# Kernel optimization log

Measured on AMD Instinct MI355X. Metric: run time of the kernel, lower is better.

The kernel has to match this reference:

```python
import jax, jax.numpy as jnp
import numpy as np

N, E, F, H, C, K = 100000, 1600000, 512, 256, 64, 10
EPS = 1e-5  # BatchNorm1d default eps


def setup_inputs() -> dict:
    key = jax.random.key(0)
    ks = jax.random.split(key, 8)
    x = jax.random.normal(ks[0], (N, F), jnp.float32)
    # edge list with no self-loops (gcn_norm adds the self-loops itself)
    src = jax.random.randint(ks[1], (E,), 0, N)
    off = jax.random.randint(ks[2], (E,), 1, N)
    dst = (src + off) % N
    edge_index = jnp.stack([src, dst])
    s = lambda k, sh: jax.random.normal(k, sh, jnp.float32) * 0.02
    W0 = s(ks[3], (F, H)); b0 = jnp.zeros((H,), jnp.float32)
    g0 = jnp.ones((H,), jnp.float32); be0 = jnp.zeros((H,), jnp.float32)
    W1 = s(ks[4], (H, H)); b1 = jnp.zeros((H,), jnp.float32)
    g1 = jnp.ones((H,), jnp.float32); be1 = jnp.zeros((H,), jnp.float32)
    W2 = s(ks[5], (H, C)); b2 = jnp.zeros((C,), jnp.float32)
    proj_w = s(ks[6], (C, 1)); proj_b = jnp.zeros((1,), jnp.float32)
    return dict(x=x, W0=W0, b0=b0, g0=g0, be0=be0, W1=W1, b1=b1, g1=g1,
                be1=be1, W2=W2, b2=b2, proj_w=proj_w, proj_b=proj_b,
                edge_index=edge_index)


def _batchnorm(h, gamma, beta):
    # training-mode BN over the node (batch) axis, biased variance like torch
    mu = h.mean(0)
    var = h.var(0)
    return gamma * (h - mu) * jax.lax.rsqrt(var + EPS) + beta


def _prop(x, edge_index, proj_w, proj_b):
    n, c = x.shape
    loop = jnp.arange(n, dtype=edge_index.dtype)
    row = jnp.concatenate([edge_index[0], loop])  # message sources (x_j)
    col = jnp.concatenate([edge_index[1], loop])  # aggregation targets
    w = jnp.ones(row.shape, x.dtype)
    deg = jax.ops.segment_sum(w, col, num_segments=n)
    dis = jnp.where(deg > 0, jax.lax.rsqrt(jnp.maximum(deg, 1.0)) * (deg > 0), 0.0)
    dis = jnp.where(deg > 0, deg ** -0.5, 0.0)
    norm = dis[row] * dis[col]  # symmetric GCN normalization per edge

    def hop(xk, _):
        msgs = norm[:, None] * xk[row]               # gather + scale  [E+N, C]
        xk = jax.ops.segment_sum(msgs, col, num_segments=n)  # scatter-add
        return xk, xk

    _, hops = jax.lax.scan(hop, x, None, length=K)   # [K, N, C]
    pps = jnp.concatenate([x[None], hops], axis=0).transpose(1, 0, 2)  # [N, K+1, C]
    score = jax.nn.sigmoid(pps @ proj_w + proj_b)[..., 0]  # [N, K+1]
    return jnp.einsum('nk,nkc->nc', score, pps)      # [N, C]


def reference(x, W0, b0, g0, be0, W1, b1, g1, be1, W2, b2, proj_w, proj_b,
              edge_index):
    h = jax.nn.relu(_batchnorm(x @ W0 + b0, g0, be0))   # dropout is identity (eval)
    h = jax.nn.relu(_batchnorm(h @ W1 + b1, g1, be1))
    h = h @ W2 + b2                                     # [N, C] logits
    out = _prop(h, edge_index, proj_w, proj_b)
    return jax.nn.log_softmax(out, axis=1)
```

## Files before the change

### kernel.cpp

```cpp
#include <hip/hip_runtime.h>
#include <hip/hip_bf16.h>
#include <math.h>

#define NN 100000
#define FF 512
#define HH 256
#define CC 64
#define KHOPS 10
#define BN_EPS 1e-5f

typedef __bf16 bf16x8 __attribute__((ext_vector_type(8)));
typedef float f32x4 __attribute__((ext_vector_type(4)));
typedef unsigned short ushort8v __attribute__((ext_vector_type(8)));

__device__ __forceinline__ unsigned short f2bf(float f) {
    __bf16 b = (__bf16)f;
    return __builtin_bit_cast(unsigned short, b);
}
__device__ __forceinline__ float bf2f(unsigned short h) {
    unsigned u = ((unsigned)h) << 16;
    return __builtin_bit_cast(float, u);
}

typedef __attribute__((address_space(1))) const void g_void;
typedef __attribute__((address_space(3))) void l_void;
__device__ __forceinline__ void gl2lds16(const void* g, void* l) {
    __builtin_amdgcn_global_load_lds((g_void*)g, (l_void*)l, 16, 0, 0);
}

__global__ void k_zero(float* p, int n) {
    int i = blockIdx.x * blockDim.x + threadIdx.x;
    if (i < n) p[i] = 0.f;
}

__global__ void k_deg_init(int* deg, int n) {
    int i = blockIdx.x * blockDim.x + threadIdx.x;
    if (i < n) deg[i] = 1;
}

__global__ void k_deg_count(const int* __restrict__ dst, int e, int* deg) {
    for (int i = blockIdx.x * blockDim.x + threadIdx.x; i < e; i += gridDim.x * blockDim.x)
        atomicAdd(&deg[dst[i]], 1);
}

__global__ void k_dis(const int* __restrict__ deg, float* dis, int n) {
    int i = blockIdx.x * blockDim.x + threadIdx.x;
    if (i < n) dis[i] = rsqrtf((float)deg[i]);
}

#define SCAN_B 1024
#define SCAN_NB ((NN + SCAN_B - 1) / SCAN_B)

__global__ void k_scan1(const int* __restrict__ deg, int* __restrict__ part, int n) {
    __shared__ int ls[SCAN_B];
    int i = blockIdx.x * SCAN_B + threadIdx.x;
    ls[threadIdx.x] = (i < n) ? deg[i] - 1 : 0;
    __syncthreads();
    for (int d = SCAN_B / 2; d > 0; d >>= 1) {
        if (threadIdx.x < d) ls[threadIdx.x] += ls[threadIdx.x + d];
        __syncthreads();
    }
    if (threadIdx.x == 0) part[blockIdx.x] = ls[0];
}

__global__ void k_scan2(int* part, int* offs_last, int nb) {
    if (threadIdx.x == 0) {
        int run = 0;
        for (int b = 0; b < nb; b++) { int v = part[b]; part[b] = run; run += v; }
        offs_last[0] = run;
    }
}

__global__ void k_scan3(const int* __restrict__ deg, const int* __restrict__ part,
                        int* __restrict__ offs, int* __restrict__ cur, int n) {
    __shared__ int ls[SCAN_B];
    int i = blockIdx.x * SCAN_B + threadIdx.x;
    int v = (i < n) ? deg[i] - 1 : 0;
    ls[threadIdx.x] = v;
    __syncthreads();
    for (int d = 1; d < SCAN_B; d <<= 1) {
        int t = (threadIdx.x >= d) ? ls[threadIdx.x - d] : 0;
        __syncthreads();
        ls[threadIdx.x] += t;
        __syncthreads();
    }
    if (i < n) {
        int ex = part[blockIdx.x] + ls[threadIdx.x] - v;
        offs[i] = ex;
        cur[i] = ex;
    }
}

__global__ void k_fill(const int* __restrict__ src, const int* __restrict__ dst, int e,
                       const float* __restrict__ dis, int* cursor,
                       int* __restrict__ csrc, float* __restrict__ cw) {
    for (int i = blockIdx.x * blockDim.x + threadIdx.x; i < e; i += gridDim.x * blockDim.x) {
        int d = dst[i];
        int s = src[i];
        int p = atomicAdd(&cursor[d], 1);
        csrc[p] = s;
        cw[p] = dis[s] * dis[d];
    }
}

__global__ void k_wt(const float* __restrict__ W, unsigned short* __restrict__ Wt,
                     int K, int N) {
    int i = blockIdx.x * blockDim.x + threadIdx.x;
    if (i < K * N) {
        int n = i / K;
        int k = i - n * K;
        Wt[i] = f2bf(W[(size_t)k * N + n]);
    }
}

template <int AF32, int BN_, int STATS>
__global__ __launch_bounds__(256) void k_gemm_mfma(
    const void* __restrict__ Av, const unsigned short* __restrict__ Bt,
    const float* __restrict__ bias, unsigned short* __restrict__ Cb,
    float* __restrict__ sum, float* __restrict__ sumsq,
    int M, int K, int Nd) {
    constexpr int NREP = BN_ / 32;
    constexpr int ACH = AF32 ? 8 : 4;
    constexpr int AOPS = AF32 ? 4 : 2;
    constexpr int ASZ = AF32 ? 16384 : 8192;
    __shared__ __align__(16) unsigned char Asb[ASZ];
    __shared__ __align__(16) unsigned char Bsb[BN_ * 64];
    const int tid = threadIdx.x;
    const int lane = tid & 63;
    const int wid = tid >> 6;
    const int wrow = wid >> 1, wcol = wid & 1;
    const int row_base = blockIdx.y * 128;
    const int col_base = blockIdx.x * BN_;
    const unsigned char* Abase = (const unsigned char*)Av;
    const size_t arowb = (size_t)K * (AF32 ? 4 : 2);

    f32x4 acc[4][NREP];
#pragma unroll
    for (int m = 0; m < 4; m++)
#pragma unroll
        for (int n = 0; n < NREP; n++)
#pragma unroll
            for (int j = 0; j < 4; j++) acc[m][n][j] = 0.f;

    for (int kt = 0; kt < K; kt += 32) {
#pragma unroll
        for (int i = 0; i < AOPS; ++i) {
            int e = i * 256 + tid;
            int r = e / ACH;
            int c = e % ACH;
            int cs = AF32 ? (c ^ (r & 7)) : (c ^ ((r >> 1) & 3));
            int grow = row_base + r;
            if (grow > M - 1) grow = M - 1;
            const void* g = Abase + (size_t)grow * arowb + (size_t)kt * (AF32 ? 4 : 2) + (cs << 4);
            gl2lds16(g, Asb + e * 16);
        }
#pragma unroll
        for (int i = 0; i < BN_ / 64; ++i) {
            int e = i * 256 + tid;
            int r = e >> 2, c = e & 3;
            int cs = c ^ ((r >> 1) & 3);
            const void* g = (const unsigned char*)Bt + (size_t)(col_base + r) * (K * 2) +
                            (size_t)kt * 2 + (cs << 4);
            gl2lds16(g, Bsb + e * 16);
        }
        __syncthreads();

        bf16x8 af[4], bfr[NREP];
#pragma unroll
        for (int m = 0; m < 4; ++m) {
            int r = wrow * 64 + m * 16 + (lane & 15);
            if (AF32) {
                int x7 = r & 7;
                int q2 = (lane >> 4) * 2;
                f32x4 f0 = *(const f32x4*)(Asb + r * 128 + ((q2 ^ x7) << 4));
                f32x4 f1 = *(const f32x4*)(Asb + r * 128 + (((q2 + 1) ^ x7) << 4));
                bf16x8 a;
                a[0] = (__bf16)f0[0]; a[1] = (__bf16)f0[1]; a[2] = (__bf16)f0[2]; a[3] = (__bf16)f0[3];
                a[4] = (__bf16)f1[0]; a[5] = (__bf16)f1[1]; a[6] = (__bf16)f1[2]; a[7] = (__bf16)f1[3];
                af[m] = a;
            } else {
                int cs = (lane >> 4) ^ ((r >> 1) & 3);
                af[m] = *(const bf16x8*)(Asb + r * 64 + (cs << 4));
            }
        }
#pragma unroll
        for (int n = 0; n < NREP; ++n) {
            int r = wcol * (BN_ / 2) + n * 16 + (lane & 15);
            int cs = (lane >> 4) ^ ((r >> 1) & 3);
            bfr[n] = *(const bf16x8*)(Bsb + r * 64 + (cs << 4));
        }
#pragma unroll
        for (int m = 0; m < 4; ++m)
#pragma unroll
            for (int n = 0; n < NREP; ++n)
                acc[m][n] = __builtin_amdgcn_mfma_f32_16x16x32_bf16(af[m], bfr[n], acc[m][n], 0, 0, 0);
        __syncthreads();
    }

    const int lc = lane & 15;
    const int lr = (lane >> 4) * 4;
#pragma unroll
    for (int m = 0; m < 4; ++m) {
        int gr0 = row_base + wrow * 64 + m * 16 + lr;
#pragma unroll
        for (int n = 0; n < NREP; ++n) {
            int gc = col_base + wcol * (BN_ / 2) + n * 16 + lc;
            float bb = bias[gc];
#pragma unroll
            for (int j = 0; j < 4; ++j) {
                int gr = gr0 + j;
                if (gr < M) Cb[(size_t)gr * Nd + gc] = f2bf(acc[m][n][j] + bb);
            }
        }
    }
    if (STATS) {
#pragma unroll
        for (int n = 0; n < NREP; ++n) {
            int gc = col_base + wcol * (BN_ / 2) + n * 16 + lc;
            float bb = bias[gc];
            float s = 0.f, s2 = 0.f;
#pragma unroll
            for (int m = 0; m < 4; ++m) {
                int gr0 = row_base + wrow * 64 + m * 16 + lr;
#pragma unroll
                for (int j = 0; j < 4; ++j) {
                    if (gr0 + j < M) {
                        float v = acc[m][n][j] + bb;
                        s += v;
                        s2 += v * v;
                    }
                }
            }
            s += __shfl_xor(s, 16); s += __shfl_xor(s, 32);
            s2 += __shfl_xor(s2, 16); s2 += __shfl_xor(s2, 32);
            if ((lane >> 4) == 0) {
                atomicAdd(&sum[gc], s);
                atomicAdd(&sumsq[gc], s2);
            }
        }
    }
}

__global__ void k_bnfin(const float* __restrict__ sum, const float* __restrict__ sq,
                        const float* __restrict__ g, const float* __restrict__ be,
                        float* scale, float* shift) {
    int c = threadIdx.x;
    float mu = sum[c] * (1.f / NN);
    float var = sq[c] * (1.f / NN) - mu * mu;
    float sc = g[c] * rsqrtf(var + BN_EPS);
    scale[c] = sc;
    shift[c] = be[c] - mu * sc;
}

__global__ void k_bnapply(unsigned short* __restrict__ h, const float* __restrict__ scale,
                          const float* __restrict__ shift, int n) {
    int total = n * 32;
    for (int idx = blockIdx.x * blockDim.x + threadIdx.x; idx < total;
         idx += gridDim.x * blockDim.x) {
        int c8 = (idx & 31) * 8;
        ushort8v v = *(ushort8v*)(h + (size_t)idx * 8);
        f32x4 s0 = *(const f32x4*)(scale + c8);
        f32x4 s1 = *(const f32x4*)(scale + c8 + 4);
        f32x4 h0 = *(const f32x4*)(shift + c8);
        f32x4 h1 = *(const f32x4*)(shift + c8 + 4);
#pragma unroll
        for (int j = 0; j < 4; j++) {
            v[j] = f2bf(fmaxf(bf2f(v[j]) * s0[j] + h0[j], 0.f));
            v[j + 4] = f2bf(fmaxf(bf2f(v[j + 4]) * s1[j] + h1[j], 0.f));
        }
        *(ushort8v*)(h + (size_t)idx * 8) = v;
    }
}

__global__ void k_hop(const unsigned short* __restrict__ xin,
                      unsigned short* __restrict__ xout,
                      const int* __restrict__ offs, const int* __restrict__ csrc,
                      const float* __restrict__ cw, const float* __restrict__ dis,
                      int n) {
    int wid = (int)((blockIdx.x * (size_t)blockDim.x + threadIdx.x) >> 6);
    if (wid >= n) return;
    int lane = threadIdx.x & 63;
    int q = lane >> 4;
    int l = lane & 15;
    const uint2* x8 = (const uint2*)xin;
    float y0 = 0.f, y1 = 0.f, y2 = 0.f, y3 = 0.f;
    if (q == 0) {
        float dn = dis[wid];
        float w = dn * dn;
        uint2 v = x8[(size_t)wid * 16 + l];
        y0 = w * bf2f((unsigned short)(v.x & 0xFFFF));
        y1 = w * bf2f((unsigned short)(v.x >> 16));
        y2 = w * bf2f((unsigned short)(v.y & 0xFFFF));
        y3 = w * bf2f((unsigned short)(v.y >> 16));
    }
    int p0 = offs[wid], p1 = offs[wid + 1];
    int p = p0 + q;
    for (; p + 4 < p1; p += 8) {
        int sA = csrc[p], sB = csrc[p + 4];
        float wA = cw[p], wB = cw[p + 4];
        uint2 vA = x8[(size_t)sA * 16 + l];
        uint2 vB = x8[(size_t)sB * 16 + l];
        y0 += wA * bf2f((unsigned short)(vA.x & 0xFFFF));
        y1 += wA * bf2f((unsigned short)(vA.x >> 16));
        y2 += wA * bf2f((unsigned short)(vA.y & 0xFFFF));
        y3 += wA * bf2f((unsigned short)(vA.y >> 16));
        y0 += wB * bf2f((unsigned short)(vB.x & 0xFFFF));
        y1 += wB * bf2f((unsigned short)(vB.x >> 16));
        y2 += wB * bf2f((unsigned short)(vB.y & 0xFFFF));
        y3 += wB * bf2f((unsigned short)(vB.y >> 16));
    }
    for (; p < p1; p += 4) {
        int s = csrc[p];
        float w = cw[p];
        uint2 v = x8[(size_t)s * 16 + l];
        y0 += w * bf2f((unsigned short)(v.x & 0xFFFF));
        y1 += w * bf2f((unsigned short)(v.x >> 16));
        y2 += w * bf2f((unsigned short)(v.y & 0xFFFF));
        y3 += w * bf2f((unsigned short)(v.y >> 16));
    }
#pragma unroll
    for (int m = 16; m <= 32; m <<= 1) {
        y0 += __shfl_xor(y0, m);
        y1 += __shfl_xor(y1, m);
        y2 += __shfl_xor(y2, m);
        y3 += __shfl_xor(y3, m);
    }
    if (q == 0) {
        uint2 r;
        r.x = ((unsigned)f2bf(y1) << 16) | (unsigned)f2bf(y0);
        r.y = ((unsigned)f2bf(y3) << 16) | (unsigned)f2bf(y2);
        ((uint2*)xout)[(size_t)wid * 16 + l] = r;
    }
}

struct XPack { const unsigned short* p[KHOPS + 1]; };

__global__ void k_finprop(XPack xp, const float* __restrict__ pw,
                          const float* __restrict__ pbp, float* __restrict__ out, int n) {
    int gw = (int)((blockIdx.x * (size_t)blockDim.x + threadIdx.x) >> 6);
    int lane = threadIdx.x & 63;
    int hf = lane >> 5;
    int l = lane & 31;
    int node = gw * 2 + hf;
    if (node >= n) return;
    float pw0 = pw[2 * l], pw1 = pw[2 * l + 1];
    float pb0 = pbp[0];
    float o0 = 0.f, o1 = 0.f;
#pragma unroll
    for (int k = 0; k <= KHOPS; k++) {
        unsigned v = ((const unsigned*)xp.p[k])[(size_t)node * 32 + l];
        float v0 = bf2f((unsigned short)(v & 0xFFFF));
        float v1 = bf2f((unsigned short)(v >> 16));
        float d = v0 * pw0 + v1 * pw1;
#pragma unroll
        for (int m = 16; m >= 1; m >>= 1) d += __shfl_xor(d, m);
        float s = 1.f / (1.f + expf(-(d + pb0)));
        o0 += s * v0;
        o1 += s * v1;
    }
    float mx = fmaxf(o0, o1);
#pragma unroll
    for (int m = 16; m >= 1; m >>= 1) mx = fmaxf(mx, __shfl_xor(mx, m));
    float e = expf(o0 - mx) + expf(o1 - mx);
#pragma unroll
    for (int m = 16; m >= 1; m >>= 1) e += __shfl_xor(e, m);
    float lg = mx + logf(e);
    float2 r = make_float2(o0 - lg, o1 - lg);
    *(float2*)(out + (size_t)node * 64 + 2 * l) = r;
}

extern "C" void kernel_launch(void* const* d_in, const int* in_sizes, int n_in,
                              void* d_out, int out_size, void* d_ws, size_t ws_size,
                              hipStream_t stream) {
    const float* x  = (const float*)d_in[0];
    const float* W0 = (const float*)d_in[1];
    const float* b0 = (const float*)d_in[2];
    const float* g0 = (const float*)d_in[3];
    const float* be0 = (const float*)d_in[4];
    const float* W1 = (const float*)d_in[5];
    const float* b1 = (const float*)d_in[6];
    const float* g1 = (const float*)d_in[7];
    const float* be1 = (const float*)d_in[8];
    const float* W2 = (const float*)d_in[9];
    const float* b2 = (const float*)d_in[10];
    const float* pw = (const float*)d_in[11];
    const float* pb = (const float*)d_in[12];
    const int* ei = (const int*)d_in[13];
    const int E = in_sizes[13] / 2;
    const int* esrc = ei;
    const int* edst = ei + E;

    char* ws = (char*)d_ws;
    const size_t XKB = (size_t)NN * CC * 2;
    unsigned short* h0b = (unsigned short*)(ws + 0);
    unsigned short* h1b = (unsigned short*)(ws + 51200000);
    unsigned short* xk[KHOPS + 1];
    xk[0] = (unsigned short*)(ws + 0);
    xk[5] = (unsigned short*)(ws + XKB);
    xk[6] = (unsigned short*)(ws + 2 * XKB);
    xk[7] = (unsigned short*)(ws + 3 * XKB);
    xk[1] = (unsigned short*)(ws + 51200000);
    xk[2] = (unsigned short*)(ws + 51200000 + XKB);
    xk[3] = (unsigned short*)(ws + 51200000 + 2 * XKB);
    xk[4] = (unsigned short*)(ws + 51200000 + 3 * XKB);
    xk[8] = (unsigned short*)(ws + 102400000);
    xk[9] = (unsigned short*)(ws + 115200000);
    xk[10] = (unsigned short*)(ws + 128000000);

    int*   deg  = (int*)  (ws + 140800000);
    float* dis  = (float*)(ws + 141200000);
    int*   offs = (int*)  (ws + 141600000);
    int*   cur  = (int*)  (ws + 142000064);
    int*   csrc = (int*)  (ws + 142400064);
    float* cw   = (float*)(ws + 148800064);
    float* stats = (float*)(ws + 155200064);
    int*   part = (int*)  (ws + 155208256);
    unsigned short* W0t = (unsigned short*)(ws + 155209280);
    unsigned short* W1t = (unsigned short*)(ws + 155471424);
    unsigned short* W2t = (unsigned short*)(ws + 155602496);

    float* sum0 = stats,        *sq0 = stats + 256;
    float* sum1 = stats + 512,  *sq1 = stats + 768;
    float* scale0 = stats + 1024, *shift0 = stats + 1280;
    float* scale1 = stats + 1536, *shift1 = stats + 1792;

    float* out = (float*)d_out;

    const int TPB = 256;
    int ngrid = (NN + TPB - 1) / TPB;
    int egrid = (E + TPB - 1) / TPB;
    int wgrid = (NN * 64 + TPB - 1) / TPB;
    int wgrid2 = (((NN + 1) / 2) * 64 + TPB - 1) / TPB;
    int mtiles = (NN + 127) / 128;

    k_zero<<<2, 1024, 0, stream>>>(stats, 2048);
    k_deg_init<<<ngrid, TPB, 0, stream>>>(deg, NN);
    k_deg_count<<<egrid, TPB, 0, stream>>>(edst, E, deg);
    k_dis<<<ngrid, TPB, 0, stream>>>(deg, dis, NN);
    k_scan1<<<SCAN_NB, SCAN_B, 0, stream>>>(deg, part, NN);
    k_scan2<<<1, 64, 0, stream>>>(part, offs + NN, SCAN_NB);
    k_scan3<<<SCAN_NB, SCAN_B, 0, stream>>>(deg, part, offs, cur, NN);
    k_fill<<<egrid, TPB, 0, stream>>>(esrc, edst, E, dis, cur, csrc, cw);

    k_wt<<<(FF * HH + TPB - 1) / TPB, TPB, 0, stream>>>(W0, W0t, FF, HH);
    k_wt<<<(HH * HH + TPB - 1) / TPB, TPB, 0, stream>>>(W1, W1t, HH, HH);
    k_wt<<<(HH * CC + TPB - 1) / TPB, TPB, 0, stream>>>(W2, W2t, HH, CC);

    k_gemm_mfma<1, 128, 1><<<dim3(HH / 128, mtiles), 256, 0, stream>>>(
        x, W0t, b0, h0b, sum0, sq0, NN, FF, HH);
    k_bnfin<<<1, 256, 0, stream>>>(sum0, sq0, g0, be0, scale0, shift0);
    k_bnapply<<<2048, TPB, 0, stream>>>(h0b, scale0, shift0, NN);

    k_gemm_mfma<0, 128, 1><<<dim3(HH / 128, mtiles), 256, 0, stream>>>(
        h0b, W1t, b1, h1b, sum1, sq1, NN, HH, HH);
    k_bnfin<<<1, 256, 0, stream>>>(sum1, sq1, g1, be1, scale1, shift1);
    k_bnapply<<<2048, TPB, 0, stream>>>(h1b, scale1, shift1, NN);

    k_gemm_mfma<0, 64, 0><<<dim3(1, mtiles), 256, 0, stream>>>(
        h1b, W2t, b2, xk[0], nullptr, nullptr, NN, HH, CC);

    for (int k = 0; k < KHOPS; k++)
        k_hop<<<wgrid, TPB, 0, stream>>>(xk[k], xk[k + 1], offs, csrc, cw, dis, NN);

    XPack xp;
    for (int k = 0; k <= KHOPS; k++) xp.p[k] = xk[k];
    k_finprop<<<wgrid2, TPB, 0, stream>>>(xp, pw, pb, out, NN);
}
```

Measured before the change: 954.4 us.

## Widen GEMM tiles to full hidden width and use 16-byte gathers in hop

The first two GEMMs now use 8-wave 512-thread blocks covering all 256 output columns, so each row of x or h is read from global memory once instead of once per column block. The hop kernel switches from 16 lanes reading 8 bytes each to 8 lanes reading 16 bytes each, which lets 8 neighbor edges be processed per wave step instead of 4. The trade-offs are higher register and LDS pressure per GEMM block, fewer blocks in flight, and more shuffle reductions per node.

```diff
diff --git a/kernel.cpp b/kernel.cpp
--- a/kernel.cpp
+++ b/kernel.cpp
@@ -20,6 +20,11 @@
 __device__ __forceinline__ float bf2f(unsigned short h) {
     unsigned u = ((unsigned)h) << 16;
     return __builtin_bit_cast(float, u);
+}
+__device__ __forceinline__ float lo16(unsigned u) { return bf2f((unsigned short)(u & 0xFFFF)); }
+__device__ __forceinline__ float hi16(unsigned u) { return bf2f((unsigned short)(u >> 16)); }
+__device__ __forceinline__ unsigned pk(float a, float b) {
+    return ((unsigned)f2bf(b) << 16) | (unsigned)f2bf(a);
 }
 
 typedef __attribute__((address_space(1))) const void g_void;
@@ -113,22 +118,26 @@
     }
 }
 
-template <int AF32, int BN_, int STATS>
-__global__ __launch_bounds__(256) void k_gemm_mfma(
+template <int AF32, int BN_, int STATS, int NW>
+__global__ __launch_bounds__(NW * 64) void k_gemm_mfma(
     const void* __restrict__ Av, const unsigned short* __restrict__ Bt,
     const float* __restrict__ bias, unsigned short* __restrict__ Cb,
     float* __restrict__ sum, float* __restrict__ sumsq,
     int M, int K, int Nd) {
-    constexpr int NREP = BN_ / 32;
+    constexpr int NT = NW * 64;
+    constexpr int WC = (NW == 8) ? 4 : 2;
+    constexpr int PWN = BN_ / WC;
+    constexpr int NREP = PWN / 16;
     constexpr int ACH = AF32 ? 8 : 4;
-    constexpr int AOPS = AF32 ? 4 : 2;
+    constexpr int AOPS = 128 * ACH / NT;
+    constexpr int BOPS = BN_ * 4 / NT;
     constexpr int ASZ = AF32 ? 16384 : 8192;
     __shared__ __align__(16) unsigned char Asb[ASZ];
     __shared__ __align__(16) unsigned char Bsb[BN_ * 64];
     const int tid = threadIdx.x;
     const int lane = tid & 63;
     const int wid = tid >> 6;
-    const int wrow = wid >> 1, wcol = wid & 1;
+    const int wrow = wid / WC, wcol = wid % WC;
     const int row_base = blockIdx.y * 128;
     const int col_base = blockIdx.x * BN_;
     const unsigned char* Abase = (const unsigned char*)Av;
@@ -145,7 +154,7 @@
     for (int kt = 0; kt < K; kt += 32) {
 #pragma unroll
         for (int i = 0; i < AOPS; ++i) {
-            int e = i * 256 + tid;
+            int e = i * NT + tid;
             int r = e / ACH;
             int c = e % ACH;
             int cs = AF32 ? (c ^ (r & 7)) : (c ^ ((r >> 1) & 3));
@@ -155,8 +164,8 @@
             gl2lds16(g, Asb + e * 16);
         }
 #pragma unroll
-        for (int i = 0; i < BN_ / 64; ++i) {
-            int e = i * 256 + tid;
+        for (int i = 0; i < BOPS; ++i) {
+            int e = i * NT + tid;
             int r = e >> 2, c = e & 3;
             int cs = c ^ ((r >> 1) & 3);
             const void* g = (const unsigned char*)Bt + (size_t)(col_base + r) * (K * 2) +
@@ -185,7 +194,7 @@
         }
 #pragma unroll
         for (int n = 0; n < NREP; ++n) {
-            int r = wcol * (BN_ / 2) + n * 16 + (lane & 15);
+            int r = wcol * PWN + n * 16 + (lane & 15);
             int cs = (lane >> 4) ^ ((r >> 1) & 3);
             bfr[n] = *(const bf16x8*)(Bsb + r * 64 + (cs << 4));
         }
@@ -204,7 +213,7 @@
         int gr0 = row_base + wrow * 64 + m * 16 + lr;
 #pragma unroll
         for (int n = 0; n < NREP; ++n) {
-            int gc = col_base + wcol * (BN_ / 2) + n * 16 + lc;
+            int gc = col_base + wcol * PWN + n * 16 + lc;
             float bb = bias[gc];
 #pragma unroll
             for (int j = 0; j < 4; ++j) {
@@ -216,7 +225,7 @@
     if (STATS) {
 #pragma unroll
         for (int n = 0; n < NREP; ++n) {
-            int gc = col_base + wcol * (BN_ / 2) + n * 16 + lc;
+            int gc = col_base + wcol * PWN + n * 16 + lc;
             float bb = bias[gc];
             float s = 0.f, s2 = 0.f;
 #pragma unroll
@@ -280,56 +289,55 @@
     int wid = (int)((blockIdx.x * (size_t)blockDim.x + threadIdx.x) >> 6);
     if (wid >= n) return;
     int lane = threadIdx.x & 63;
-    int q = lane >> 4;
-    int l = lane & 15;
-    const uint2* x8 = (const uint2*)xin;
-    float y0 = 0.f, y1 = 0.f, y2 = 0.f, y3 = 0.f;
-    if (q == 0) {
+    int g = lane >> 3;
+    int j = lane & 7;
+    const uint4* x16 = (const uint4*)xin;
+    float y0 = 0.f, y1 = 0.f, y2 = 0.f, y3 = 0.f, y4 = 0.f, y5 = 0.f, y6 = 0.f, y7 = 0.f;
+    if (g == 0) {
         float dn = dis[wid];
         float w = dn * dn;
-        uint2 v = x8[(size_t)wid * 16 + l];
-        y0 = w * bf2f((unsigned short)(v.x & 0xFFFF));
-        y1 = w * bf2f((unsigned short)(v.x >> 16));
-        y2 = w * bf2f((unsigned short)(v.y & 0xFFFF));
-        y3 = w * bf2f((unsigned short)(v.y >> 16));
+        uint4 v = x16[(size_t)wid * 8 + j];
+        y0 = w * lo16(v.x); y1 = w * hi16(v.x);
+        y2 = w * lo16(v.y); y3 = w * hi16(v.y);
+        y4 = w * lo16(v.z); y5 = w * hi16(v.z);
+        y6 = w * lo16(v.w); y7 = w * hi16(v.w);
     }
     int p0 = offs[wid], p1 = offs[wid + 1];
-    int p = p0 + q;
-    for (; p + 4 < p1; p += 8) {
-        int sA = csrc[p], sB = csrc[p + 4];
-        float wA = cw[p], wB = cw[p + 4];
-        uint2 vA = x8[(size_t)sA * 16 + l];
-        uint2 vB = x8[(size_t)sB * 16 + l];
-        y0 += wA * bf2f((unsigned short)(vA.x & 0xFFFF));
-        y1 += wA * bf2f((unsigned short)(vA.x >> 16));
-        y2 += wA * bf2f((unsigned short)(vA.y & 0xFFFF));
-        y3 += wA * bf2f((unsigned short)(vA.y >> 16));
-        y0 += wB * bf2f((unsigned short)(vB.x & 0xFFFF));
-        y1 += wB * bf2f((unsigned short)(vB.x >> 16));
-        y2 += wB * bf2f((unsigned short)(vB.y & 0xFFFF));
-        y3 += wB * bf2f((unsigned short)(vB.y >> 16));
-    }
-    for (; p < p1; p += 4) {
+    int p = p0 + g;
+    for (; p + 8 < p1; p += 16) {
+        int sA = csrc[p], sB = csrc[p + 8];
+        float wA = cw[p], wB = cw[p + 8];
+        uint4 vA = x16[(size_t)sA * 8 + j];
+        uint4 vB = x16[(size_t)sB * 8 + j];
+        y0 += wA * lo16(vA.x); y1 += wA * hi16(vA.x);
+        y2 += wA * lo16(vA.y); y3 += wA * hi16(vA.y);
+        y4 += wA * lo16(vA.z); y5 += wA * hi16(vA.z);
+        y6 += wA * lo16(vA.w); y7 += wA * hi16(vA.w);
+        y0 += wB * lo16(vB.x); y1 += wB * hi16(vB.x);
+        y2 += wB * lo16(vB.y); y3 += wB * hi16(vB.y);
+        y4 += wB * lo16(vB.z); y5 += wB * hi16(vB.z);
+        y6 += wB * lo16(vB.w); y7 += wB * hi16(vB.w);
+    }
+    for (; p < p1; p += 8) {
         int s = csrc[p];
         float w = cw[p];
-        uint2 v = x8[(size_t)s * 16 + l];
-        y0 += w * bf2f((unsigned short)(v.x & 0xFFFF));
-        y1 += w * bf2f((unsigned short)(v.x >> 16));
-        y2 += w * bf2f((unsigned short)(v.y & 0xFFFF));
-        y3 += w * bf2f((unsigned short)(v.y >> 16));
-    }
-#pragma unroll
-    for (int m = 16; m <= 32; m <<= 1) {
-        y0 += __shfl_xor(y0, m);
-        y1 += __shfl_xor(y1, m);
-        y2 += __shfl_xor(y2, m);
-        y3 += __shfl_xor(y3, m);
-    }
-    if (q == 0) {
-        uint2 r;
-        r.x = ((unsigned)f2bf(y1) << 16) | (unsigned)f2bf(y0);
-        r.y = ((unsigned)f2bf(y3) << 16) | (unsigned)f2bf(y2);
-        ((uint2*)xout)[(size_t)wid * 16 + l] = r;
+        uint4 v = x16[(size_t)s * 8 + j];
+        y0 += w * lo16(v.x); y1 += w * hi16(v.x);
+        y2 += w * lo16(v.y); y3 += w * hi16(v.y);
+        y4 += w * lo16(v.z); y5 += w * hi16(v.z);
+        y6 += w * lo16(v.w); y7 += w * hi16(v.w);
+    }
+#pragma unroll
+    for (int m = 8; m <= 32; m <<= 1) {
+        y0 += __shfl_xor(y0, m); y1 += __shfl_xor(y1, m);
+        y2 += __shfl_xor(y2, m); y3 += __shfl_xor(y3, m);
+        y4 += __shfl_xor(y4, m); y5 += __shfl_xor(y5, m);
+        y6 += __shfl_xor(y6, m); y7 += __shfl_xor(y7, m);
+    }
+    if (g == 0) {
+        uint4 r;
+        r.x = pk(y0, y1); r.y = pk(y2, y3); r.z = pk(y4, y5); r.w = pk(y6, y7);
+        ((uint4*)xout)[(size_t)wid * 8 + j] = r;
     }
 }
 
@@ -349,8 +357,8 @@
 #pragma unroll
     for (int k = 0; k <= KHOPS; k++) {
         unsigned v = ((const unsigned*)xp.p[k])[(size_t)node * 32 + l];
-        float v0 = bf2f((unsigned short)(v & 0xFFFF));
-        float v1 = bf2f((unsigned short)(v >> 16));
+        float v0 = lo16(v);
+        float v1 = hi16(v);
         float d = v0 * pw0 + v1 * pw1;
 #pragma unroll
         for (int m = 16; m >= 1; m >>= 1) d += __shfl_xor(d, m);
@@ -446,17 +454,17 @@
     k_wt<<<(HH * HH + TPB - 1) / TPB, TPB, 0, stream>>>(W1, W1t, HH, HH);
     k_wt<<<(HH * CC + TPB - 1) / TPB, TPB, 0, stream>>>(W2, W2t, HH, CC);
 
-    k_gemm_mfma<1, 128, 1><<<dim3(HH / 128, mtiles), 256, 0, stream>>>(
+    k_gemm_mfma<1, 256, 1, 8><<<dim3(1, mtiles), 512, 0, stream>>>(
         x, W0t, b0, h0b, sum0, sq0, NN, FF, HH);
     k_bnfin<<<1, 256, 0, stream>>>(sum0, sq0, g0, be0, scale0, shift0);
     k_bnapply<<<2048, TPB, 0, stream>>>(h0b, scale0, shift0, NN);
 
-    k_gemm_mfma<0, 128, 1><<<dim3(HH / 128, mtiles), 256, 0, stream>>>(
+    k_gemm_mfma<0, 256, 1, 8><<<dim3(1, mtiles), 512, 0, stream>>>(
         h0b, W1t, b1, h1b, sum1, sq1, NN, HH, HH);
     k_bnfin<<<1, 256, 0, stream>>>(sum1, sq1, g1, be1, scale1, shift1);
     k_bnapply<<<2048, TPB, 0, stream>>>(h1b, scale1, shift1, NN);
 
-    k_gemm_mfma<0, 64, 0><<<dim3(1, mtiles), 256, 0, stream>>>(
+    k_gemm_mfma<0, 64, 0, 4><<<dim3(1, mtiles), 256, 0, stream>>>(
         h1b, W2t, b2, xk[0], nullptr, nullptr, NN, HH, CC);
 
     for (int k = 0; k < KHOPS; k++)
```

Measured after the change: 887.0 us. 1.08x faster.
